# Optimization experiments

Hardware: AMD Instinct MI355X
Metric: run time of the kernel (lower is better)

The kernel has to match this reference:

```python
import jax, jax.numpy as jnp
import numpy as np

E = 128        # EMBEDDING_DIM
H = 8          # HEAD_NUM
K = 16         # KEY_DIM
NODE = 200     # NODE_SIZE
CLIP = 10.0    # LOGIT_CLIPPING
B = 256
G = 200        # group size
S = 100        # solution tokens


def setup_inputs() -> dict:
    key = jax.random.key(0)
    ks = jax.random.split(key, 9)
    sc = 1.0 / np.sqrt(E)
    return {
        "graph": jax.random.normal(ks[0], (B, 1, E), jnp.float32),
        "capacity": jax.random.uniform(ks[1], (B, G), jnp.float32),
        "sols_mask_pomo": jnp.zeros((B, G, S), jnp.float32),
        "ninf_mask": jnp.zeros((B, G, NODE), jnp.float32),
        "encoded_nodes": jax.random.normal(ks[2], (B, NODE + S, E), jnp.float32),
        "Wq": jax.random.normal(ks[3], (1 + E, H * K), jnp.float32) * sc,
        "Wk": jax.random.normal(ks[4], (E, H * K), jnp.float32) * sc,
        "Wv": jax.random.normal(ks[5], (E, H * K), jnp.float32) * sc,
        "Wc": jax.random.normal(ks[6], (H * K, E), jnp.float32) * sc,
        "bc": jax.random.normal(ks[7], (E,), jnp.float32) * sc,
        "Wk_logit": jax.random.normal(ks[8], (E, E), jnp.float32) * sc,
    }


def _heads(x):
    # [B, C, H*K] -> [B, H, C, K]
    b, c, _ = x.shape
    return x.reshape(b, c, H, K).transpose(0, 2, 1, 3)


def _mha(q, k, v, group_ninf_mask):
    # q: [B,H,n,K], k/v: [B,H,m,K], mask: [B,n,m]
    score = jnp.einsum("bhnk,bhmk->bhnm", q, k) / np.sqrt(K)
    score = score + group_ninf_mask[:, None, :, :]
    w = jax.nn.softmax(score, axis=-1)
    out = jnp.einsum("bhnm,bhmk->bhnk", w, v)          # [B,H,n,K]
    b, _, n, _ = out.shape
    return out.transpose(0, 2, 1, 3).reshape(b, n, H * K)


def reference(graph, capacity, sols_mask_pomo, ninf_mask, encoded_nodes,
              Wq, Wk, Wv, Wc, bc, Wk_logit):
    nodes, sols = encoded_nodes[:, :NODE], encoded_nodes[:, NODE:]
    # reset(): NOTE original uses Wk/Wv for solution tokens too
    k = _heads(nodes @ Wk)
    v = _heads(nodes @ Wv)
    k_s = _heads(sols @ Wk)
    v_s = _heads(sols @ Wv)
    single_head_key = nodes @ Wk_logit                   # [B, NODE, E]

    b, g = capacity.shape
    inp = jnp.concatenate(
        [jnp.broadcast_to(graph, (b, g, E)), capacity[:, :, None]], axis=2)
    q = _heads(inp @ Wq)                                 # [B,H,G,K]

    out_n = _mha(q, k, v, ninf_mask)
    out_s = _mha(q, k_s, v_s, sols_mask_pomo)
    mh = (out_n + out_s) @ Wc + bc                       # [B,G,E]

    score = jnp.einsum("bge,bne->bgn", mh, single_head_key) / np.sqrt(E)
    score = CLIP * jnp.tanh(score) + ninf_mask
    return jax.nn.softmax(score, axis=2)
```

## Files before the change

### kernel.cpp

```cpp
#include <hip/hip_runtime.h>

#define B_    256
#define G_    200
#define S_    100
#define NODE_ 200
#define E_    128
#define H_    8
#define M_    300
#define MT_   19
#define NT_   13
#define CLIP_ 10.0f

typedef float    f32x4 __attribute__((ext_vector_type(4)));
typedef short    s16x4 __attribute__((ext_vector_type(4)));
typedef short    s16x8 __attribute__((ext_vector_type(8)));
typedef unsigned u32x4 __attribute__((ext_vector_type(4)));

#define MFMA16(A, B, C) __builtin_amdgcn_mfma_f32_16x16x32_bf16(A, B, C, 0, 0, 0)

__device__ __forceinline__ unsigned bf16u(float x) {
    unsigned u = __builtin_bit_cast(unsigned, x);
    return (u + 0x7fffu + ((u >> 16) & 1u)) >> 16;
}
__device__ __forceinline__ float bfbits(unsigned hb16) {
    return __builtin_bit_cast(float, hb16 << 16);
}
__device__ __forceinline__ short bfhi(float x) { return (short)bf16u(x); }
__device__ __forceinline__ short bflo(float x, short hi) {
    float hf = __builtin_bit_cast(float, ((unsigned)(unsigned short)hi) << 16);
    return (short)bf16u(x - hf);
}
__device__ __forceinline__ unsigned cvtpk(float a, float b) {
    unsigned r;
    asm("v_cvt_pk_bf16_f32 %0, %1, %2" : "=v"(r) : "v"(a), "v"(b));
    return r;
}
__device__ __forceinline__ s16x8 cat8(s16x4 a, s16x4 b) {
    s16x8 r; r[0]=a[0]; r[1]=a[1]; r[2]=a[2]; r[3]=a[3];
             r[4]=b[0]; r[5]=b[1]; r[6]=b[2]; r[7]=b[3]; return r;
}
__device__ __forceinline__ f32x4 max4(f32x4 a, f32x4 b) {
    f32x4 r; r[0]=fmaxf(a[0],b[0]); r[1]=fmaxf(a[1],b[1]);
             r[2]=fmaxf(a[2],b[2]); r[3]=fmaxf(a[3],b[3]); return r;
}
__device__ __forceinline__ void split_pack(f32x4 v, s16x8& B1, s16x8& B2) {
    unsigned h01 = cvtpk(v[0], v[1]);
    unsigned h23 = cvtpk(v[2], v[3]);
    float e0 = v[0] - __builtin_bit_cast(float, h01 << 16);
    float e1 = v[1] - __builtin_bit_cast(float, h01 & 0xffff0000u);
    float e2 = v[2] - __builtin_bit_cast(float, h23 << 16);
    float e3 = v[3] - __builtin_bit_cast(float, h23 & 0xffff0000u);
    unsigned l01 = cvtpk(e0, e1), l23 = cvtpk(e2, e3);
    u32x4 w1 = {h01, h23, l01, l23};
    u32x4 w2 = {l01, l23, h01, h23};
    B1 = __builtin_bit_cast(s16x8, w1);
    B2 = __builtin_bit_cast(s16x8, w2);
}

__global__ __launch_bounds__(64) void wfrag_kernel(
    const float* __restrict__ Wk, const float* __restrict__ Wv,
    const float* __restrict__ Wl, const float* __restrict__ Wc,
    short* __restrict__ wf8_hi, short* __restrict__ wf8_lo)
{
    const int p = blockIdx.x, ct = blockIdx.y;
    const int l = threadIdx.x, qq = l >> 4, li = l & 15;
    const float* W = (p == 0) ? Wk : ((p == 1) ? Wv : ((p == 2) ? Wl : Wc));
    for (int kc = 0; kc < 8; ++kc) {
        s16x4 hi, lo;
        #pragma unroll
        for (int j = 0; j < 4; ++j) {
            float v = W[(kc*16 + qq*4 + j)*E_ + ct*16 + li];
            short h = bfhi(v); hi[j] = h; lo[j] = bflo(v, h);
        }
        const int ix = (((p*8 + ct)*4 + (kc >> 1))*64 + l)*8 + (kc & 1)*4;
        *(s16x4*)(wf8_hi + ix) = hi;
        *(s16x4*)(wf8_lo + ix) = lo;
    }
}

__global__ __launch_bounds__(128) void qbase_kernel(
    const float* __restrict__ graph, const float* __restrict__ Wq,
    float* __restrict__ qbase)
{
    const int b = blockIdx.x, c = threadIdx.x;
    __shared__ float gs[E_];
    gs[c] = graph[b*E_ + c];
    __syncthreads();
    float acc = 0.f;
    #pragma unroll 8
    for (int e = 0; e < E_; ++e) acc += gs[e] * Wq[e*E_ + c];
    qbase[b*E_ + c] = acc;
}

__global__ __launch_bounds__(64, 4) void proj_kernel(
    const float* __restrict__ enc,
    const short* __restrict__ wf8_hi, const short* __restrict__ wf8_lo,
    short* __restrict__ kf_il, short* __restrict__ vf_il,
    short* __restrict__ sf8_hi, short* __restrict__ sf8_lo)
{
    int id = blockIdx.x;
    { const int xcd = id & 7, pos = id >> 3; id = xcd*608 + pos; }
    const int b = id / MT_, mt = id % MT_;
    const int l = threadIdx.x, qq = l >> 4, li = l & 15;
    const int m = mt*16 + li;

    s16x8 Ahi[4], Alo[4];
    #pragma unroll
    for (int u = 0; u < 4; ++u) {
        float va[8];
        if (m < M_) {
            const float* ep = enc + ((size_t)b*M_ + m)*E_ + u*32 + qq*4;
            float4 f0 = *(const float4*)ep;
            float4 f1 = *(const float4*)(ep + 16);
            va[0]=f0.x; va[1]=f0.y; va[2]=f0.z; va[3]=f0.w;
            va[4]=f1.x; va[5]=f1.y; va[6]=f1.z; va[7]=f1.w;
        } else {
            #pragma unroll
            for (int j = 0; j < 8; ++j) va[j] = 0.f;
        }
        #pragma unroll
        for (int j = 0; j < 8; ++j) {
            short h = bfhi(va[j]); Ahi[u][j] = h; Alo[u][j] = bflo(va[j], h);
        }
    }

    __shared__ unsigned tile[16*17];

    #pragma unroll
    for (int p = 0; p < 3; ++p) {
        if (p == 2 && mt >= NT_) break;
        #pragma unroll
        for (int ct = 0; ct < 8; ++ct) {
            f32x4 acc = {0.f, 0.f, 0.f, 0.f};
            #pragma unroll
            for (int u = 0; u < 4; ++u) {
                const int base = (((p*8 + ct)*4 + u)*64 + l)*8;
                s16x8 Bh = *(const s16x8*)(wf8_hi + base);
                s16x8 Bl = *(const s16x8*)(wf8_lo + base);
                acc = MFMA16(Ahi[u], Bh, acc);
                acc = MFMA16(Ahi[u], Bl, acc);
                acc = MFMA16(Alo[u], Bh, acc);
            }
            if (p == 1) {
                s16x4 oh, ol;
                #pragma unroll
                for (int r = 0; r < 4; ++r) { short h = bfhi(acc[r]); oh[r] = h; ol[r] = bflo(acc[r], h); }
                const size_t ix = (((size_t)(b*8 + ct))*MT_ + mt)*512 + (size_t)l*8;
                *(s16x8*)(vf_il + ix) = cat8(oh, ol);
            } else {
                #pragma unroll
                for (int r = 0; r < 4; ++r) {
                    short h = bfhi(acc[r]); short lo = bflo(acc[r], h);
                    tile[(qq*4 + r)*17 + li] = (((unsigned)(unsigned short)h) << 16) | (unsigned short)(unsigned)lo;
                }
                __syncthreads();
                s16x4 oh, ol;
                #pragma unroll
                for (int j = 0; j < 4; ++j) {
                    unsigned wv = tile[li*17 + qq*4 + j];
                    oh[j] = (short)(wv >> 16); ol[j] = (short)(wv & 0xffffu);
                }
                if (p == 0) {
                    const size_t ix = (((size_t)(b*8 + ct))*MT_ + mt)*512 + (size_t)l*8;
                    *(s16x8*)(kf_il + ix) = cat8(oh, ol);
                } else {
                    const size_t ix = (((size_t)(b*NT_ + mt))*4 + (ct >> 1))*512 + (size_t)l*8 + (ct & 1)*4;
                    *(s16x4*)(sf8_hi + ix) = oh;
                    *(s16x4*)(sf8_lo + ix) = ol;
                }
                __syncthreads();
            }
        }
    }
}

__global__ __launch_bounds__(256, 3) void attn1_kernel(
    const float* __restrict__ capacity, const float* __restrict__ sols_mask,
    const float* __restrict__ ninf_mask, const float* __restrict__ Wq,
    const float* __restrict__ qbase,
    const short* __restrict__ kf_il, const short* __restrict__ vf_il,
    float* __restrict__ outws)
{
    int id = blockIdx.x;
    { const int xcd = id & 7, pos = id >> 3; id = xcd*416 + pos; }
    const int b = id / NT_, gt = id % NT_;
    const int t = threadIdx.x;
    const int w = t >> 6, l = t & 63, qq = l >> 4, li = l & 15;
    const int g0 = gt*16;

    __shared__ unsigned mlds[MT_][64][2];

    {
        const size_t bg = (size_t)b*G_;
        for (int f = t; f < 1600; f += 256) {
            const int g = f/100, p = f - g*100;
            int gg = g0 + g; gg = (gg < G_) ? gg : G_-1;
            float2 v = *(const float2*)(ninf_mask + (bg + gg)*NODE_ + p*2);
            const int mm = p*2;
            mlds[mm>>4][((mm>>2)&3)*16 + g][(mm>>1)&1] = cvtpk(v.x, v.y);
        }
        for (int f = t; f < 800; f += 256) {
            const int g = f/50, p = f - g*50;
            int gg = g0 + g; gg = (gg < G_) ? gg : G_-1;
            float2 v = *(const float2*)(sols_mask + (bg + gg)*S_ + p*2);
            const int mm = 200 + p*2;
            mlds[mm>>4][((mm>>2)&3)*16 + g][(mm>>1)&1] = cvtpk(v.x, v.y);
        }
        if (t < 32) {
            const unsigned nu = bf16u(-3.0e38f);
            mlds[18][48 + (t>>1)][t&1] = nu | (nu << 16);
        }
    }
    __syncthreads();

    int ggl = g0 + li; ggl = (ggl < G_) ? ggl : G_-1;
    const float cap = capacity[b*G_ + ggl];
    const bool isN12 = (qq < 2);

    #pragma unroll 1
    for (int hi2 = 0; hi2 < 2; ++hi2) {
        const int h = w*2 + hi2;
        s16x8 qB1, qB2;
        {
            float4 qb4 = *(const float4*)(qbase + b*E_ + h*16 + qq*4);
            float4 wl4 = *(const float4*)(Wq + E_*E_ + h*16 + qq*4);
            f32x4 qv = {qb4.x + cap*wl4.x, qb4.y + cap*wl4.y,
                        qb4.z + cap*wl4.z, qb4.w + cap*wl4.w};
            split_pack(qv, qB1, qB2);
        }
        f32x4 sc[MT_];
        const size_t kb = ((size_t)(b*8 + h)*MT_)*512 + (size_t)l*8;
        #pragma unroll
        for (int mt = 0; mt < MT_; ++mt) {
            s16x8 kf8 = *(const s16x8*)(kf_il + kb + (size_t)mt*512);
            f32x4 a = {0.f, 0.f, 0.f, 0.f};
            a = MFMA16(kf8, qB1, a);
            a = MFMA16(kf8, qB2, a);
            sc[mt] = a;
        }
        #pragma unroll
        for (int mt = 0; mt < MT_; ++mt) {
            uint2 mp = *(const uint2*)&mlds[mt][l][0];
            sc[mt][0] = sc[mt][0]*0.25f + bfbits(mp.x & 0xffffu);
            sc[mt][1] = sc[mt][1]*0.25f + bfbits(mp.x >> 16);
            sc[mt][2] = sc[mt][2]*0.25f + bfbits(mp.y & 0xffffu);
            sc[mt][3] = sc[mt][3]*0.25f + bfbits(mp.y >> 16);
        }
        float mxN, mxS;
        {
            f32x4 a0 = max4(sc[0], sc[1]),  a1 = max4(sc[2], sc[3]),  a2 = max4(sc[4], sc[5]);
            f32x4 a3 = max4(sc[6], sc[7]),  a4 = max4(sc[8], sc[9]),  a5 = max4(sc[10], sc[11]);
            f32x4 mN4 = max4(max4(max4(a0, a1), max4(a2, a3)), max4(a4, a5));
            f32x4 s0 = max4(sc[13], sc[14]), s1 = max4(sc[15], sc[16]), s2 = max4(sc[17], sc[18]);
            f32x4 mS4 = max4(max4(s0, s1), s2);
            mxN = fmaxf(fmaxf(mN4[0], mN4[1]), fmaxf(mN4[2], mN4[3]));
            mxS = fmaxf(fmaxf(mS4[0], mS4[1]), fmaxf(mS4[2], mS4[3]));
            float t12 = fmaxf(fmaxf(sc[12][0], sc[12][1]), fmaxf(sc[12][2], sc[12][3]));
            if (isN12) mxN = fmaxf(mxN, t12); else mxS = fmaxf(mxS, t12);
            mxN = fmaxf(mxN, __shfl_xor(mxN, 16)); mxN = fmaxf(mxN, __shfl_xor(mxN, 32));
            mxS = fmaxf(mxS, __shfl_xor(mxS, 16)); mxS = fmaxf(mxS, __shfl_xor(mxS, 32));
        }
        float sN, sS;
        {
            f32x4 sA = {0.f,0.f,0.f,0.f}, sB = {0.f,0.f,0.f,0.f}, sC = {0.f,0.f,0.f,0.f};
            #pragma unroll
            for (int mt = 0; mt < 12; mt += 2) {
                f32x4 e0, e1;
                #pragma unroll
                for (int r = 0; r < 4; ++r) { e0[r] = __expf(sc[mt][r]   - mxN);
                                              e1[r] = __expf(sc[mt+1][r] - mxN); }
                sc[mt] = e0; sc[mt+1] = e1; sA += e0; sB += e1;
            }
            #pragma unroll
            for (int mt = 13; mt < MT_; ++mt) {
                f32x4 e;
                #pragma unroll
                for (int r = 0; r < 4; ++r) e[r] = __expf(sc[mt][r] - mxS);
                sc[mt] = e; sC += e;
            }
            const float mx12 = isN12 ? mxN : mxS;
            float s12 = 0.f;
            #pragma unroll
            for (int r = 0; r < 4; ++r) { float e = __expf(sc[12][r] - mx12); sc[12][r] = e; s12 += e; }
            f32x4 sAB = sA + sB;
            sN = (sAB[0] + sAB[1]) + (sAB[2] + sAB[3]) + (isN12 ? s12 : 0.f);
            sS = (sC[0] + sC[1]) + (sC[2] + sC[3]) + (isN12 ? 0.f : s12);
            sN += __shfl_xor(sN, 16); sN += __shfl_xor(sN, 32);
            sS += __shfl_xor(sS, 16); sS += __shfl_xor(sS, 32);
        }
        const float rN = 1.f / sN, rS = 1.f / sS;
        #pragma unroll
        for (int mt = 0; mt < 12; ++mt) sc[mt] *= rN;
        { const float r12 = isN12 ? rN : rS; sc[12] *= r12; }
        #pragma unroll
        for (int mt = 13; mt < MT_; ++mt) sc[mt] *= rS;

        f32x4 oacc[4] = {{0.f,0.f,0.f,0.f},{0.f,0.f,0.f,0.f},
                         {0.f,0.f,0.f,0.f},{0.f,0.f,0.f,0.f}};
        #pragma unroll
        for (int mt = 0; mt < MT_; ++mt) {
            s16x8 pB1, pB2;
            split_pack(sc[mt], pB1, pB2);
            s16x8 vf8 = *(const s16x8*)(vf_il + kb + (size_t)mt*512);
            oacc[mt & 3] = MFMA16(vf8, pB1, oacc[mt & 3]);
            oacc[mt & 3] = MFMA16(vf8, pB2, oacc[mt & 3]);
        }
        f32x4 osum = (oacc[0] + oacc[1]) + (oacc[2] + oacc[3]);
        *(f32x4*)(outws + (((size_t)(b*NT_ + gt))*8 + h)*256 + (size_t)l*4) = osum;
    }
}

__global__ __launch_bounds__(64, 4) void attn2_kernel(
    const float* __restrict__ ninf_mask,
    const short* __restrict__ sf8_hi, const short* __restrict__ sf8_lo,
    const short* __restrict__ wf8_hi, const short* __restrict__ wf8_lo,
    const float* __restrict__ bc_,
    const float* __restrict__ outws,
    float* __restrict__ out)
{
    int id = blockIdx.x;
    { const int xcd = id & 7, pos = id >> 3; id = xcd*416 + pos; }
    const int b = id / NT_, gt = id % NT_;
    const int l = threadIdx.x, qq = l >> 4, li = l & 15;
    const int g0 = gt*16;

    __shared__ float pool[16*308];

    {
        const size_t bg = (size_t)b*G_;
        for (int f = l; f < 800; f += 64) {
            const int g = f/50, p = f - g*50;
            int gg = g0 + g; gg = (gg < G_) ? gg : G_-1;
            *(float4*)&pool[g*308 + p*4] = *(const float4*)(ninf_mask + (bg + gg)*NODE_ + p*4);
        }
    }
    __syncthreads();

    s16x8 BhO[4], BlO[4];
    #pragma unroll
    for (int u = 0; u < 4; ++u) {
        f32x4 a0 = *(const f32x4*)(outws + (((size_t)(b*NT_ + gt))*8 + 2*u)*256 + (size_t)l*4);
        f32x4 a1 = *(const f32x4*)(outws + (((size_t)(b*NT_ + gt))*8 + 2*u + 1)*256 + (size_t)l*4);
        unsigned ha = cvtpk(a0[0], a0[1]), hb = cvtpk(a0[2], a0[3]);
        unsigned hc = cvtpk(a1[0], a1[1]), hd = cvtpk(a1[2], a1[3]);
        float e0 = a0[0] - __builtin_bit_cast(float, ha << 16);
        float e1 = a0[1] - __builtin_bit_cast(float, ha & 0xffff0000u);
        float e2 = a0[2] - __builtin_bit_cast(float, hb << 16);
        float e3 = a0[3] - __builtin_bit_cast(float, hb & 0xffff0000u);
        float e4 = a1[0] - __builtin_bit_cast(float, hc << 16);
        float e5 = a1[1] - __builtin_bit_cast(float, hc & 0xffff0000u);
        float e6 = a1[2] - __builtin_bit_cast(float, hd << 16);
        float e7 = a1[3] - __builtin_bit_cast(float, hd & 0xffff0000u);
        unsigned la = cvtpk(e0, e1), lb = cvtpk(e2, e3);
        unsigned lc = cvtpk(e4, e5), ld = cvtpk(e6, e7);
        u32x4 wh = {ha, hb, hc, hd}, wl = {la, lb, lc, ld};
        BhO[u] = __builtin_bit_cast(s16x8, wh);
        BlO[u] = __builtin_bit_cast(s16x8, wl);
    }
    s16x8 Bh2[4], Bl2[4];
    #pragma unroll
    for (int u = 0; u < 4; ++u) {
        f32x4 t01[2];
        #pragma unroll
        for (int half = 0; half < 2; ++half) {
            const int jt = 2*u + half;
            f32x4 acc = {0.f, 0.f, 0.f, 0.f};
            #pragma unroll
            for (int uu = 0; uu < 4; ++uu) {
                const int base = (((3*8 + jt)*4 + uu)*64 + l)*8;
                s16x8 Ah = *(const s16x8*)(wf8_hi + base);
                s16x8 Al = *(const s16x8*)(wf8_lo + base);
                acc = MFMA16(Ah, BhO[uu], acc);
                acc = MFMA16(Ah, BlO[uu], acc);
                acc = MFMA16(Al, BhO[uu], acc);
            }
            float4 b4 = *(const float4*)(bc_ + jt*16 + qq*4);
            acc[0] += b4.x; acc[1] += b4.y; acc[2] += b4.z; acc[3] += b4.w;
            t01[half] = acc;
        }
        unsigned h0 = cvtpk(t01[0][0], t01[0][1]), h1 = cvtpk(t01[0][2], t01[0][3]);
        unsigned h2 = cvtpk(t01[1][0], t01[1][1]), h3 = cvtpk(t01[1][2], t01[1][3]);
        float e0 = t01[0][0] - __builtin_bit_cast(float, h0 << 16);
        float e1 = t01[0][1] - __builtin_bit_cast(float, h0 & 0xffff0000u);
        float e2 = t01[0][2] - __builtin_bit_cast(float, h1 << 16);
        float e3 = t01[0][3] - __builtin_bit_cast(float, h1 & 0xffff0000u);
        float e4 = t01[1][0] - __builtin_bit_cast(float, h2 << 16);
        float e5 = t01[1][1] - __builtin_bit_cast(float, h2 & 0xffff0000u);
        float e6 = t01[1][2] - __builtin_bit_cast(float, h3 << 16);
        float e7 = t01[1][3] - __builtin_bit_cast(float, h3 & 0xffff0000u);
        unsigned l0 = cvtpk(e0, e1), l1 = cvtpk(e2, e3);
        unsigned l2 = cvtpk(e4, e5), l3 = cvtpk(e6, e7);
        u32x4 wh = {h0, h1, h2, h3}, wl = {l0, l1, l2, l3};
        Bh2[u] = __builtin_bit_cast(s16x8, wh);
        Bl2[u] = __builtin_bit_cast(s16x8, wl);
    }
    f32x4 z[NT_];
    #pragma unroll
    for (int nt = 0; nt < NT_; ++nt) {
        f32x4 acc = {0.f, 0.f, 0.f, 0.f};
        #pragma unroll
        for (int u = 0; u < 4; ++u) {
            const size_t base = (((size_t)(b*NT_ + nt))*4 + u)*512 + (size_t)l*8;
            s16x8 Ah = *(const s16x8*)(sf8_hi + base);
            s16x8 Al = *(const s16x8*)(sf8_lo + base);
            acc = MFMA16(Ah, Bh2[u], acc);
            acc = MFMA16(Ah, Bl2[u], acc);
            acc = MFMA16(Al, Bh2[u], acc);
        }
        z[nt] = acc;
    }
    const float rE = 0.08838834764831845f;
    #pragma unroll
    for (int nt = 0; nt < NT_; ++nt) {
        f32x4 mk = *(const f32x4*)&pool[li*308 + nt*16 + qq*4];
        #pragma unroll
        for (int r = 0; r < 4; ++r) {
            float lg;
            if (nt < 12 || (qq*4 + r) < 8) {
                float a2 = z[nt][r] * rE;
                float ex = __expf(2.f * a2);
                float th = 1.f - 2.f / (ex + 1.f);
                lg = CLIP_*th + mk[r];
            } else lg = -3.0e38f;
            z[nt][r] = lg;
        }
    }
    float mx;
    {
        f32x4 m0 = max4(z[0], z[1]),  m1 = max4(z[2], z[3]),  m2 = max4(z[4], z[5]);
        f32x4 m3 = max4(z[6], z[7]),  m4 = max4(z[8], z[9]),  m5 = max4(z[10], z[11]);
        f32x4 mm = max4(max4(max4(m0, m1), max4(m2, m3)), max4(max4(m4, m5), z[12]));
        mx = fmaxf(fmaxf(mm[0], mm[1]), fmaxf(mm[2], mm[3]));
        mx = fmaxf(mx, __shfl_xor(mx, 16)); mx = fmaxf(mx, __shfl_xor(mx, 32));
    }
    float sm;
    {
        f32x4 sA = {0.f,0.f,0.f,0.f}, sB = {0.f,0.f,0.f,0.f};
        #pragma unroll
        for (int nt = 0; nt < 12; nt += 2) {
            f32x4 e0, e1;
            #pragma unroll
            for (int r = 0; r < 4; ++r) { e0[r] = __expf(z[nt][r]   - mx);
                                          e1[r] = __expf(z[nt+1][r] - mx); }
            z[nt] = e0; z[nt+1] = e1; sA += e0; sB += e1;
        }
        f32x4 e;
        #pragma unroll
        for (int r = 0; r < 4; ++r) e[r] = __expf(z[12][r] - mx);
        z[12] = e; sA += e;
        f32x4 sAB = sA + sB;
        sm = (sAB[0] + sAB[1]) + (sAB[2] + sAB[3]);
        sm += __shfl_xor(sm, 16); sm += __shfl_xor(sm, 32);
    }
    const float rs = 1.f / sm;

    float* ob = out + (size_t)b*G_*NODE_;
    __syncthreads();
    #pragma unroll
    for (int ch = 0; ch < 4; ++ch) {
        const int ntn = (ch < 3) ? 4 : 1;
        for (int k = 0; k < ntn; ++k) {
            const int nt = ch*4 + k;
            #pragma unroll
            for (int r = 0; r < 4; ++r)
                pool[li*69 + k*16 + qq*4 + r] = z[nt][r] * rs;
        }
        __syncthreads();
        const int n = ch*64 + l;
        const bool nok = (ch < 3) || (l < 8);
        #pragma unroll
        for (int gi = 0; gi < 16; ++gi) {
            const int g = g0 + gi;
            if (nok && g < G_) ob[(size_t)g*NODE_ + n] = pool[gi*69 + l];
        }
        __syncthreads();
    }
}

extern "C" void kernel_launch(void* const* d_in, const int* in_sizes, int n_in,
                              void* d_out, int out_size, void* d_ws, size_t ws_size,
                              hipStream_t stream) {
    (void)in_sizes; (void)n_in; (void)out_size; (void)ws_size;
    const float* graph = (const float*)d_in[0];
    const float* capacity = (const float*)d_in[1];
    const float* sols_mask = (const float*)d_in[2];
    const float* ninf_mask = (const float*)d_in[3];
    const float* enc = (const float*)d_in[4];
    const float* Wq  = (const float*)d_in[5];
    const float* Wk  = (const float*)d_in[6];
    const float* Wv  = (const float*)d_in[7];
    const float* Wc  = (const float*)d_in[8];
    const float* bc  = (const float*)d_in[9];
    const float* Wkl = (const float*)d_in[10];
    float* out = (float*)d_out;

    char* wsb = (char*)d_ws;
    short* kf_il  = (short*)(wsb);
    short* sf8_hi = (short*)(wsb + 39845888);
    short* sf8_lo = (short*)(wsb + 53477376);
    short* wf8_hi = (short*)(wsb + 67108864);
    short* wf8_lo = (short*)(wsb + 67239936);
    float* qb     = (float*)(wsb + 67371008);
    float* outws  = (float*)(wsb + 67502080);
    short* vf_il  = (short*)d_out;

    wfrag_kernel<<<dim3(4, 8), 64, 0, stream>>>(Wk, Wv, Wkl, Wc, wf8_hi, wf8_lo);
    qbase_kernel<<<B_, 128, 0, stream>>>(graph, Wq, qb);
    proj_kernel<<<MT_*B_, 64, 0, stream>>>(enc, wf8_hi, wf8_lo, kf_il, vf_il, sf8_hi, sf8_lo);
    attn1_kernel<<<NT_*B_, 256, 0, stream>>>(capacity, sols_mask, ninf_mask, Wq, qb,
                                             kf_il, vf_il, outws);
    attn2_kernel<<<NT_*B_, 64, 0, stream>>>(ninf_mask, sf8_hi, sf8_lo, wf8_hi, wf8_lo,
                                            bc, outws, out);
}
```

Measured before the change: 190.5 us.

## Fuse attention and logit stages into one kernel, drop softmax max pass

```diff
diff --git a/kernel.cpp b/kernel.cpp
--- a/kernel.cpp
+++ b/kernel.cpp
@@ -9,7 +9,6 @@
 #define M_    300
 #define MT_   19
 #define NT_   13
-#define CLIP_ 10.0f
 
 typedef float    f32x4 __attribute__((ext_vector_type(4)));
 typedef short    s16x4 __attribute__((ext_vector_type(4)));
@@ -18,6 +17,11 @@
 
 #define MFMA16(A, B, C) __builtin_amdgcn_mfma_f32_16x16x32_bf16(A, B, C, 0, 0, 0)
 
+#define LOG2E_  1.4426950408889634f
+#define CQ_     0.36067376022224085f
+#define C2T_    0.25503901628148863f
+#define C10L_   14.426950408889634f
+
 __device__ __forceinline__ unsigned bf16u(float x) {
     unsigned u = __builtin_bit_cast(unsigned, x);
     return (u + 0x7fffu + ((u >> 16) & 1u)) >> 16;
@@ -33,6 +37,11 @@
 __device__ __forceinline__ unsigned cvtpk(float a, float b) {
     unsigned r;
     asm("v_cvt_pk_bf16_f32 %0, %1, %2" : "=v"(r) : "v"(a), "v"(b));
+    return r;
+}
+__device__ __forceinline__ float exp2a(float x) {
+    float r;
+    asm("v_exp_f32 %0, %1" : "=v"(r) : "v"(x));
     return r;
 }
 __device__ __forceinline__ s16x8 cat8(s16x4 a, s16x4 b) {
@@ -55,6 +64,23 @@
     u32x4 w2 = {l01, l23, h01, h23};
     B1 = __builtin_bit_cast(s16x8, w1);
     B2 = __builtin_bit_cast(s16x8, w2);
+}
+__device__ __forceinline__ void pack8(f32x4 a0, f32x4 a1, s16x8& Bh, s16x8& Bl) {
+    unsigned ha = cvtpk(a0[0], a0[1]), hb = cvtpk(a0[2], a0[3]);
+    unsigned hc = cvtpk(a1[0], a1[1]), hd = cvtpk(a1[2], a1[3]);
+    float e0 = a0[0] - __builtin_bit_cast(float, ha << 16);
+    float e1 = a0[1] - __builtin_bit_cast(float, ha & 0xffff0000u);
+    float e2 = a0[2] - __builtin_bit_cast(float, hb << 16);
+    float e3 = a0[3] - __builtin_bit_cast(float, hb & 0xffff0000u);
+    float e4 = a1[0] - __builtin_bit_cast(float, hc << 16);
+    float e5 = a1[1] - __builtin_bit_cast(float, hc & 0xffff0000u);
+    float e6 = a1[2] - __builtin_bit_cast(float, hd << 16);
+    float e7 = a1[3] - __builtin_bit_cast(float, hd & 0xffff0000u);
+    unsigned la = cvtpk(e0, e1), lb = cvtpk(e2, e3);
+    unsigned lc = cvtpk(e4, e5), ld = cvtpk(e6, e7);
+    u32x4 wh = {ha, hb, hc, hd}, wl = {la, lb, lc, ld};
+    Bh = __builtin_bit_cast(s16x8, wh);
+    Bl = __builtin_bit_cast(s16x8, wl);
 }
 
 __global__ __launch_bounds__(64) void wfrag_kernel(
@@ -174,12 +200,17 @@
     }
 }
 
-__global__ __launch_bounds__(256, 3) void attn1_kernel(
+template <int FUSED>
+__global__ __launch_bounds__(256, 3) void attn_fused_kernel(
     const float* __restrict__ capacity, const float* __restrict__ sols_mask,
     const float* __restrict__ ninf_mask, const float* __restrict__ Wq,
     const float* __restrict__ qbase,
     const short* __restrict__ kf_il, const short* __restrict__ vf_il,
-    float* __restrict__ outws)
+    const short* __restrict__ wf8_hi, const short* __restrict__ wf8_lo,
+    const short* __restrict__ sf8_hi, const short* __restrict__ sf8_lo,
+    const float* __restrict__ bc_,
+    float* __restrict__ outws,
+    float* __restrict__ out)
 {
     int id = blockIdx.x;
     { const int xcd = id & 7, pos = id >> 3; id = xcd*416 + pos; }
@@ -189,6 +220,10 @@
     const int g0 = gt*16;
 
     __shared__ unsigned mlds[MT_][64][2];
+    __shared__ float out_l[8*64*4];
+    __shared__ float zbuf[16*212];
+    __shared__ float ps[64];
+    __shared__ float rsl[16];
 
     {
         const size_t bg = (size_t)b*G_;
@@ -197,18 +232,17 @@
             int gg = g0 + g; gg = (gg < G_) ? gg : G_-1;
             float2 v = *(const float2*)(ninf_mask + (bg + gg)*NODE_ + p*2);
             const int mm = p*2;
-            mlds[mm>>4][((mm>>2)&3)*16 + g][(mm>>1)&1] = cvtpk(v.x, v.y);
+            mlds[mm>>4][((mm>>2)&3)*16 + g][(mm>>1)&1] = cvtpk(v.x*LOG2E_, v.y*LOG2E_);
         }
         for (int f = t; f < 800; f += 256) {
             const int g = f/50, p = f - g*50;
             int gg = g0 + g; gg = (gg < G_) ? gg : G_-1;
             float2 v = *(const float2*)(sols_mask + (bg + gg)*S_ + p*2);
             const int mm = 200 + p*2;
-            mlds[mm>>4][((mm>>2)&3)*16 + g][(mm>>1)&1] = cvtpk(v.x, v.y);
+            mlds[mm>>4][((mm>>2)&3)*16 + g][(mm>>1)&1] = cvtpk(v.x*LOG2E_, v.y*LOG2E_);
         }
         if (t < 32) {
-            const unsigned nu = bf16u(-3.0e38f);
-            mlds[18][48 + (t>>1)][t&1] = nu | (nu << 16);
+            mlds[18][48 + (t>>1)][t&1] = 0xFF80FF80u;
         }
     }
     __syncthreads();
@@ -238,75 +272,133 @@
             a = MFMA16(kf8, qB2, a);
             sc[mt] = a;
         }
+        f32x4 sA = {0.f,0.f,0.f,0.f}, sB = {0.f,0.f,0.f,0.f}, sC = {0.f,0.f,0.f,0.f};
         #pragma unroll
         for (int mt = 0; mt < MT_; ++mt) {
-            uint2 mp = *(const uint2*)&mlds[mt][l][0];
-            sc[mt][0] = sc[mt][0]*0.25f + bfbits(mp.x & 0xffffu);
-            sc[mt][1] = sc[mt][1]*0.25f + bfbits(mp.x >> 16);
-            sc[mt][2] = sc[mt][2]*0.25f + bfbits(mp.y & 0xffffu);
-            sc[mt][3] = sc[mt][3]*0.25f + bfbits(mp.y >> 16);
-        }
-        float mxN, mxS;
-        {
-            f32x4 a0 = max4(sc[0], sc[1]),  a1 = max4(sc[2], sc[3]),  a2 = max4(sc[4], sc[5]);
-            f32x4 a3 = max4(sc[6], sc[7]),  a4 = max4(sc[8], sc[9]),  a5 = max4(sc[10], sc[11]);
-            f32x4 mN4 = max4(max4(max4(a0, a1), max4(a2, a3)), max4(a4, a5));
-            f32x4 s0 = max4(sc[13], sc[14]), s1 = max4(sc[15], sc[16]), s2 = max4(sc[17], sc[18]);
-            f32x4 mS4 = max4(max4(s0, s1), s2);
-            mxN = fmaxf(fmaxf(mN4[0], mN4[1]), fmaxf(mN4[2], mN4[3]));
-            mxS = fmaxf(fmaxf(mS4[0], mS4[1]), fmaxf(mS4[2], mS4[3]));
-            float t12 = fmaxf(fmaxf(sc[12][0], sc[12][1]), fmaxf(sc[12][2], sc[12][3]));
-            if (isN12) mxN = fmaxf(mxN, t12); else mxS = fmaxf(mxS, t12);
-            mxN = fmaxf(mxN, __shfl_xor(mxN, 16)); mxN = fmaxf(mxN, __shfl_xor(mxN, 32));
-            mxS = fmaxf(mxS, __shfl_xor(mxS, 16)); mxS = fmaxf(mxS, __shfl_xor(mxS, 32));
-        }
-        float sN, sS;
-        {
-            f32x4 sA = {0.f,0.f,0.f,0.f}, sB = {0.f,0.f,0.f,0.f}, sC = {0.f,0.f,0.f,0.f};
-            #pragma unroll
-            for (int mt = 0; mt < 12; mt += 2) {
-                f32x4 e0, e1;
-                #pragma unroll
-                for (int r = 0; r < 4; ++r) { e0[r] = __expf(sc[mt][r]   - mxN);
-                                              e1[r] = __expf(sc[mt+1][r] - mxN); }
-                sc[mt] = e0; sc[mt+1] = e1; sA += e0; sB += e1;
-            }
-            #pragma unroll
-            for (int mt = 13; mt < MT_; ++mt) {
-                f32x4 e;
-                #pragma unroll
-                for (int r = 0; r < 4; ++r) e[r] = __expf(sc[mt][r] - mxS);
-                sc[mt] = e; sC += e;
-            }
-            const float mx12 = isN12 ? mxN : mxS;
-            float s12 = 0.f;
-            #pragma unroll
-            for (int r = 0; r < 4; ++r) { float e = __expf(sc[12][r] - mx12); sc[12][r] = e; s12 += e; }
-            f32x4 sAB = sA + sB;
-            sN = (sAB[0] + sAB[1]) + (sAB[2] + sAB[3]) + (isN12 ? s12 : 0.f);
-            sS = (sC[0] + sC[1]) + (sC[2] + sC[3]) + (isN12 ? 0.f : s12);
-            sN += __shfl_xor(sN, 16); sN += __shfl_xor(sN, 32);
-            sS += __shfl_xor(sS, 16); sS += __shfl_xor(sS, 32);
-        }
+            const uint2 mp = *(const uint2*)&mlds[mt][l][0];
+            f32x4 e;
+            e[0] = exp2a(fmaf(sc[mt][0], CQ_, bfbits(mp.x & 0xffffu)));
+            e[1] = exp2a(fmaf(sc[mt][1], CQ_, bfbits(mp.x >> 16)));
+            e[2] = exp2a(fmaf(sc[mt][2], CQ_, bfbits(mp.y & 0xffffu)));
+            e[3] = exp2a(fmaf(sc[mt][3], CQ_, bfbits(mp.y >> 16)));
+            sc[mt] = e;
+            if (mt < 12)       { if (mt & 1) sB += e; else sA += e; }
+            else if (mt > 12)  sC += e;
+        }
+        float s12 = (sc[12][0] + sc[12][1]) + (sc[12][2] + sc[12][3]);
+        f32x4 sAB = sA + sB;
+        float sN = (sAB[0] + sAB[1]) + (sAB[2] + sAB[3]) + (isN12 ? s12 : 0.f);
+        float sS = (sC[0] + sC[1]) + (sC[2] + sC[3]) + (isN12 ? 0.f : s12);
+        sN += __shfl_xor(sN, 16); sN += __shfl_xor(sN, 32);
+        sS += __shfl_xor(sS, 16); sS += __shfl_xor(sS, 32);
         const float rN = 1.f / sN, rS = 1.f / sS;
-        #pragma unroll
-        for (int mt = 0; mt < 12; ++mt) sc[mt] *= rN;
         { const float r12 = isN12 ? rN : rS; sc[12] *= r12; }
-        #pragma unroll
-        for (int mt = 13; mt < MT_; ++mt) sc[mt] *= rS;
-
-        f32x4 oacc[4] = {{0.f,0.f,0.f,0.f},{0.f,0.f,0.f,0.f},
-                         {0.f,0.f,0.f,0.f},{0.f,0.f,0.f,0.f}};
+
+        f32x4 oN0 = {0.f,0.f,0.f,0.f}, oN1 = {0.f,0.f,0.f,0.f};
+        f32x4 oS0 = {0.f,0.f,0.f,0.f}, oS1 = {0.f,0.f,0.f,0.f};
+        f32x4 o12 = {0.f,0.f,0.f,0.f};
         #pragma unroll
         for (int mt = 0; mt < MT_; ++mt) {
             s16x8 pB1, pB2;
             split_pack(sc[mt], pB1, pB2);
             s16x8 vf8 = *(const s16x8*)(vf_il + kb + (size_t)mt*512);
-            oacc[mt & 3] = MFMA16(vf8, pB1, oacc[mt & 3]);
-            oacc[mt & 3] = MFMA16(vf8, pB2, oacc[mt & 3]);
-        }
-        f32x4 osum = (oacc[0] + oacc[1]) + (oacc[2] + oacc[3]);
-        *(f32x4*)(outws + (((size_t)(b*NT_ + gt))*8 + h)*256 + (size_t)l*4) = osum;
+            f32x4& acc = (mt < 12) ? ((mt & 1) ? oN1 : oN0)
+                       : (mt == 12 ? o12 : ((mt & 1) ? oS1 : oS0));
+            acc = MFMA16(vf8, pB1, acc);
+            acc = MFMA16(vf8, pB2, acc);
+        }
+        f32x4 on = oN0 + oN1, os = oS0 + oS1, osum;
+        #pragma unroll
+        for (int r = 0; r < 4; ++r)
+            osum[r] = fmaf(on[r], rN, fmaf(os[r], rS, o12[r]));
+
+        if (FUSED) {
+            *(f32x4*)(out_l + (h*64 + l)*4) = osum;
+        } else {
+            *(f32x4*)(outws + (((size_t)(b*NT_ + gt))*8 + h)*256 + (size_t)l*4) = osum;
+        }
+    }
+
+    if constexpr (FUSED) {
+        __syncthreads();
+        s16x8 BhO[4], BlO[4];
+        #pragma unroll
+        for (int u = 0; u < 4; ++u) {
+            f32x4 a0 = *(const f32x4*)(out_l + ((2*u)*64 + l)*4);
+            f32x4 a1 = *(const f32x4*)(out_l + ((2*u + 1)*64 + l)*4);
+            pack8(a0, a1, BhO[u], BlO[u]);
+        }
+        f32x4 mh01[2];
+        #pragma unroll
+        for (int half = 0; half < 2; ++half) {
+            const int jt = w*2 + half;
+            f32x4 acc = {0.f, 0.f, 0.f, 0.f};
+            #pragma unroll
+            for (int uu = 0; uu < 4; ++uu) {
+                const int base = (((3*8 + jt)*4 + uu)*64 + l)*8;
+                s16x8 Ah = *(const s16x8*)(wf8_hi + base);
+                s16x8 Al = *(const s16x8*)(wf8_lo + base);
+                acc = MFMA16(Ah, BhO[uu], acc);
+                acc = MFMA16(Ah, BlO[uu], acc);
+                acc = MFMA16(Al, BhO[uu], acc);
+            }
+            float4 b4 = *(const float4*)(bc_ + jt*16 + qq*4);
+            acc[0] += b4.x; acc[1] += b4.y; acc[2] += b4.z; acc[3] += b4.w;
+            mh01[half] = acc;
+        }
+        __syncthreads();
+        *(f32x4*)(out_l + ((w*2)*64 + l)*4)     = mh01[0];
+        *(f32x4*)(out_l + ((w*2 + 1)*64 + l)*4) = mh01[1];
+        __syncthreads();
+
+        s16x8 Bh2[4], Bl2[4];
+        #pragma unroll
+        for (int u = 0; u < 4; ++u) {
+            f32x4 m0 = *(const f32x4*)(out_l + ((2*u)*64 + l)*4);
+            f32x4 m1 = *(const f32x4*)(out_l + ((2*u + 1)*64 + l)*4);
+            pack8(m0, m1, Bh2[u], Bl2[u]);
+        }
+        float psum = 0.f;
+        for (int i = 0; i < 4; ++i) {
+            const int nt = w + 4*i;
+            if (nt >= NT_) break;
+            f32x4 acc = {0.f, 0.f, 0.f, 0.f};
+            #pragma unroll
+            for (int u = 0; u < 4; ++u) {
+                const size_t base = (((size_t)(b*NT_ + nt))*4 + u)*512 + (size_t)l*8;
+                s16x8 Ah = *(const s16x8*)(sf8_hi + base);
+                s16x8 Al = *(const s16x8*)(sf8_lo + base);
+                acc = MFMA16(Ah, Bh2[u], acc);
+                acc = MFMA16(Ah, Bl2[u], acc);
+                acc = MFMA16(Al, Bh2[u], acc);
+            }
+            const uint2 mp = *(const uint2*)&mlds[nt][l][0];
+            f32x4 ev;
+            {
+                float ex0 = exp2a(acc[0]*C2T_), ex1 = exp2a(acc[1]*C2T_);
+                float ex2 = exp2a(acc[2]*C2T_), ex3 = exp2a(acc[3]*C2T_);
+                float th0 = 1.f - 2.f/(ex0 + 1.f), th1 = 1.f - 2.f/(ex1 + 1.f);
+                float th2 = 1.f - 2.f/(ex2 + 1.f), th3 = 1.f - 2.f/(ex3 + 1.f);
+                ev[0] = exp2a(fmaf(th0, C10L_, bfbits(mp.x & 0xffffu)));
+                ev[1] = exp2a(fmaf(th1, C10L_, bfbits(mp.x >> 16)));
+                ev[2] = exp2a(fmaf(th2, C10L_, bfbits(mp.y & 0xffffu)));
+                ev[3] = exp2a(fmaf(th3, C10L_, bfbits(mp.y >> 16)));
+            }
+            if (nt == 12 && qq >= 2) { ev[0]=0.f; ev[1]=0.f; ev[2]=0.f; ev[3]=0.f; }
+            *(f32x4*)(zbuf + li*212 + nt*16 + qq*4) = ev;
+            psum += (ev[0] + ev[1]) + (ev[2] + ev[3]);
+        }
+        psum += __shfl_xor(psum, 16); psum += __shfl_xor(psum, 32);
+        if (qq == 0) ps[w*16 + li] = psum;
+        __syncthreads();
+        if (t < 16) rsl[t] = 1.f / (ps[t] + ps[16 + t] + ps[32 + t] + ps[48 + t]);
+        __syncthreads();
+
+        float* ob = out + ((size_t)b*G_ + g0)*NODE_;
+        for (int g2 = 0; g2 < 16; ++g2) {
+            if (g0 + g2 < G_ && t < NODE_)
+                ob[(size_t)g2*NODE_ + t] = zbuf[g2*212 + t] * rsl[g2];
+        }
     }
 }
 
@@ -341,21 +433,7 @@
     for (int u = 0; u < 4; ++u) {
         f32x4 a0 = *(const f32x4*)(outws + (((size_t)(b*NT_ + gt))*8 + 2*u)*256 + (size_t)l*4);
         f32x4 a1 = *(const f32x4*)(outws + (((size_t)(b*NT_ + gt))*8 + 2*u + 1)*256 + (size_t)l*4);
-        unsigned ha = cvtpk(a0[0], a0[1]), hb = cvtpk(a0[2], a0[3]);
-        unsigned hc = cvtpk(a1[0], a1[1]), hd = cvtpk(a1[2], a1[3]);
-        float e0 = a0[0] - __builtin_bit_cast(float, ha << 16);
-        float e1 = a0[1] - __builtin_bit_cast(float, ha & 0xffff0000u);
-        float e2 = a0[2] - __builtin_bit_cast(float, hb << 16);
-        float e3 = a0[3] - __builtin_bit_cast(float, hb & 0xffff0000u);
-        float e4 = a1[0] - __builtin_bit_cast(float, hc << 16);
-        float e5 = a1[1] - __builtin_bit_cast(float, hc & 0xffff0000u);
-        float e6 = a1[2] - __builtin_bit_cast(float, hd << 16);
-        float e7 = a1[3] - __builtin_bit_cast(float, hd & 0xffff0000u);
-        unsigned la = cvtpk(e0, e1), lb = cvtpk(e2, e3);
-        unsigned lc = cvtpk(e4, e5), ld = cvtpk(e6, e7);
-        u32x4 wh = {ha, hb, hc, hd}, wl = {la, lb, lc, ld};
-        BhO[u] = __builtin_bit_cast(s16x8, wh);
-        BlO[u] = __builtin_bit_cast(s16x8, wl);
+        pack8(a0, a1, BhO[u], BlO[u]);
     }
     s16x8 Bh2[4], Bl2[4];
     #pragma unroll
@@ -378,21 +456,7 @@
             acc[0] += b4.x; acc[1] += b4.y; acc[2] += b4.z; acc[3] += b4.w;
             t01[half] = acc;
         }
-        unsigned h0 = cvtpk(t01[0][0], t01[0][1]), h1 = cvtpk(t01[0][2], t01[0][3]);
-        unsigned h2 = cvtpk(t01[1][0], t01[1][1]), h3 = cvtpk(t01[1][2], t01[1][3]);
-        float e0 = t01[0][0] - __builtin_bit_cast(float, h0 << 16);
-        float e1 = t01[0][1] - __builtin_bit_cast(float, h0 & 0xffff0000u);
-        float e2 = t01[0][2] - __builtin_bit_cast(float, h1 << 16);
-        float e3 = t01[0][3] - __builtin_bit_cast(float, h1 & 0xffff0000u);
-        float e4 = t01[1][0] - __builtin_bit_cast(float, h2 << 16);
-        float e5 = t01[1][1] - __builtin_bit_cast(float, h2 & 0xffff0000u);
-        float e6 = t01[1][2] - __builtin_bit_cast(float, h3 << 16);
-        float e7 = t01[1][3] - __builtin_bit_cast(float, h3 & 0xffff0000u);
-        unsigned l0 = cvtpk(e0, e1), l1 = cvtpk(e2, e3);
-        unsigned l2 = cvtpk(e4, e5), l3 = cvtpk(e6, e7);
-        u32x4 wh = {h0, h1, h2, h3}, wl = {l0, l1, l2, l3};
-        Bh2[u] = __builtin_bit_cast(s16x8, wh);
-        Bl2[u] = __builtin_bit_cast(s16x8, wl);
+        pack8(t01[0], t01[1], Bh2[u], Bl2[u]);
     }
     f32x4 z[NT_];
     #pragma unroll
@@ -420,7 +484,7 @@
                 float a2 = z[nt][r] * rE;
                 float ex = __expf(2.f * a2);
                 float th = 1.f - 2.f / (ex + 1.f);
-                lg = CLIP_*th + mk[r];
+                lg = 10.f*th + mk[r];
             } else lg = -3.0e38f;
             z[nt][r] = lg;
         }
@@ -480,7 +544,7 @@
 extern "C" void kernel_launch(void* const* d_in, const int* in_sizes, int n_in,
                               void* d_out, int out_size, void* d_ws, size_t ws_size,
                               hipStream_t stream) {
-    (void)in_sizes; (void)n_in; (void)out_size; (void)ws_size;
+    (void)in_sizes; (void)n_in; (void)out_size;
     const float* graph = (const float*)d_in[0];
     const float* capacity = (const float*)d_in[1];
     const float* sols_mask = (const float*)d_in[2];
@@ -501,14 +565,22 @@
     short* wf8_hi = (short*)(wsb + 67108864);
     short* wf8_lo = (short*)(wsb + 67239936);
     float* qb     = (float*)(wsb + 67371008);
+    const bool fused = (ws_size >= 107347968ull);
+    short* vf_il  = fused ? (short*)(wsb + 67502080) : (short*)d_out;
     float* outws  = (float*)(wsb + 67502080);
-    short* vf_il  = (short*)d_out;
 
     wfrag_kernel<<<dim3(4, 8), 64, 0, stream>>>(Wk, Wv, Wkl, Wc, wf8_hi, wf8_lo);
     qbase_kernel<<<B_, 128, 0, stream>>>(graph, Wq, qb);
     proj_kernel<<<MT_*B_, 64, 0, stream>>>(enc, wf8_hi, wf8_lo, kf_il, vf_il, sf8_hi, sf8_lo);
-    attn1_kernel<<<NT_*B_, 256, 0, stream>>>(capacity, sols_mask, ninf_mask, Wq, qb,
-                                             kf_il, vf_il, outws);
-    attn2_kernel<<<NT_*B_, 64, 0, stream>>>(ninf_mask, sf8_hi, sf8_lo, wf8_hi, wf8_lo,
-                                            bc, outws, out);
-}
+    if (fused) {
+        attn_fused_kernel<1><<<NT_*B_, 256, 0, stream>>>(
+            capacity, sols_mask, ninf_mask, Wq, qb, kf_il, vf_il,
+            wf8_hi, wf8_lo, sf8_hi, sf8_lo, bc, nullptr, out);
+    } else {
+        attn_fused_kernel<0><<<NT_*B_, 256, 0, stream>>>(
+            capacity, sols_mask, ninf_mask, Wq, qb, kf_il, vf_il,
+            wf8_hi, wf8_lo, sf8_hi, sf8_lo, bc, outws, nullptr);
+        attn2_kernel<<<NT_*B_, 64, 0, stream>>>(ninf_mask, sf8_hi, sf8_lo,
+                                                wf8_hi, wf8_lo, bc, outws, out);
+    }
+}
```

After: 203.9 us. +7.1%, slower.
